# Performance work log

Hardware: AMD Instinct MI355X
Metric: run time of the kernel (lower is better)

## Reference

```python
import jax, jax.numpy as jnp
import numpy as np

D = 300      # d_model / entity_embed_size, hard-coded in the module
TOPK = 20    # k in torch.topk


def setup_inputs() -> dict:
    key = jax.random.key(0)
    ks = jax.random.split(key, 6)
    N, T = 2, 4096
    scale = 1.0 / np.sqrt(D).astype(np.float32)
    return {
        "querys": jax.random.normal(ks[0], (N, T, D), jnp.float32),
        "keys":   jax.random.normal(ks[1], (N, T, D), jnp.float32),
        "values": jax.random.normal(ks[2], (N, T, D), jnp.float32),
        "Wq": jax.random.normal(ks[3], (D, D), jnp.float32) * scale,
        "Wk": jax.random.normal(ks[4], (D, D), jnp.float32) * scale,
        "Wv": jax.random.normal(ks[5], (D, D), jnp.float32) * scale,
        "num_heads": 6,
    }


def reference(querys, keys, values, Wq, Wk, Wv, num_heads):
    N, Tq, d = querys.shape
    h = int(num_heads)
    dh = d // h  # head dim (must divide; 300/6 = 50)

    # nn.Linear(bias=False): y = x @ W^T
    Q = querys @ Wq.T
    K = keys @ Wk.T
    V = values @ Wv.T  # computed but unused by the 'selected' attention, kept for fidelity

    # torch.cat(torch.split(X, dh, dim=2), dim=0): head index becomes major batch dim
    def to_heads(X):
        n, t, _ = X.shape
        return X.reshape(n, t, h, dh).transpose(2, 0, 1, 3).reshape(h * n, t, dh)

    Q_, K_ = to_heads(Q), to_heads(K)

    # scaled_dot_selected_product_attention
    scores = jnp.einsum('bqd,bkd->bqk', Q_, K_) / (dh ** 0.5)  # [hN, Tq, Tk]
    max_att = scores.max(axis=1)                                # [hN, Tk] (max over queries)
    top_vals, top_ids = jax.lax.top_k(max_att, TOPK)            # [hN, 20]
    probs = jax.nn.softmax(top_vals, axis=-1)                   # [hN, 20]
    # gather from K (not V!), matching the original code
    sel = jnp.take_along_axis(K_, top_ids[:, :, None], axis=1)  # [hN, 20, dh]
    out = jnp.sum(sel * probs[:, :, None], axis=1, keepdims=True)  # [hN, 1, dh]

    # torch.cat(torch.split(outputs, N, dim=0), dim=2): merge heads back on feature dim
    out = out.reshape(h, N, 1, dh).transpose(1, 2, 0, 3).reshape(N, 1, d)
    return out
```

## Files before the change

kernel.cpp:

```cpp
#include <hip/hip_runtime.h>
#include <hip/hip_bf16.h>
#include <math.h>

#define T      4096
#define Dm     300
#define NH     6
#define DH     50
#define NB     2
#define NBATCH 12
#define KTOP   20
#define NCAND  48
#define QC     8
#define RQC    16
#define KP     320
#define JP     320
#define NBINS  4096
#define BMAX   1024
#define XCHUNKS (16384 * 40)
#define WCHUNKS (2 * JP * (KP / 8))

typedef short  bs8  __attribute__((ext_vector_type(8)));
typedef float  f4   __attribute__((ext_vector_type(4)));

static __device__ __forceinline__ unsigned short f2bf(float f) {
    union { float f; unsigned u; } x{f};
    unsigned r = x.u + 0x7fffu + ((x.u >> 16) & 1u);
    return (unsigned short)(r >> 16);
}
static __device__ __forceinline__ float bf2f(unsigned short h) {
    union { unsigned u; float f; } x;
    x.u = ((unsigned)h) << 16;
    return x.f;
}
static __device__ __forceinline__ unsigned fkey(float f) {
    unsigned u = __float_as_uint(f);
    return (u & 0x80000000u) ? ~u : (u | 0x80000000u);
}

__global__ __launch_bounds__(256) void split_kernel(
    const float* __restrict__ querys, const float* __restrict__ keys,
    const float* __restrict__ Wq, const float* __restrict__ Wk,
    unsigned short* __restrict__ Xh, unsigned short* __restrict__ Xl,
    unsigned short* __restrict__ Wh, unsigned short* __restrict__ Wl)
{
    const int i = blockIdx.x * 256 + threadIdx.x;
    float f[8];
    unsigned short *dh, *dl;

    if (i < XCHUNKS) {
        int row = i / 40, c = i - row * 40;
        int k0 = c * 8;
        int z = row >> 13, r = row & 8191;
        const float* src = (z ? keys : querys) + (size_t)r * 300;
        if (k0 + 8 <= 300) {
            float4 a = *(const float4*)(src + k0);
            float4 b = *(const float4*)(src + k0 + 4);
            f[0] = a.x; f[1] = a.y; f[2] = a.z; f[3] = a.w;
            f[4] = b.x; f[5] = b.y; f[6] = b.z; f[7] = b.w;
        } else {
#pragma unroll
            for (int e = 0; e < 8; ++e) {
                int k = k0 + e;
                f[e] = (k < 300) ? src[k < 300 ? k : 0] : 0.f;
            }
        }
        dh = Xh + (size_t)row * KP + k0;
        dl = Xl + (size_t)row * KP + k0;
    } else if (i < XCHUNKS + WCHUNKS) {
        int wi = i - XCHUNKS;
        int z = wi / (JP * (KP / 8)), rem = wi % (JP * (KP / 8));
        int row = rem / (KP / 8), k0 = (rem % (KP / 8)) * 8;
        const float* W = z ? Wk : Wq;
#pragma unroll
        for (int e = 0; e < 8; ++e) {
            int k = k0 + e;
            f[e] = (row < 300 && k < 300) ? W[row * 300 + (k < 300 ? k : 0)] : 0.f;
        }
        dh = Wh + ((size_t)z * JP + row) * KP + k0;
        dl = Wl + ((size_t)z * JP + row) * KP + k0;
    } else {
        return;
    }

    bs8 vh, vl;
#pragma unroll
    for (int e = 0; e < 8; ++e) {
        unsigned short h = f2bf(f[e]);
        float r = f[e] - bf2f(h);
        vh[e] = (short)h;
        vl[e] = (short)f2bf(r);
    }
    *(bs8*)dh = vh;
    *(bs8*)dl = vl;
}

__global__ __launch_bounds__(256) void proj_mfma_kernel(
    const unsigned short* __restrict__ Xh, const unsigned short* __restrict__ Xl,
    const unsigned short* __restrict__ Wh, const unsigned short* __restrict__ Wl,
    float* __restrict__ Qt, float* __restrict__ Kt)
{
    __shared__ unsigned short Bfh[1280 * 8];
    __shared__ unsigned short Bfl[1280 * 8];

    const int z  = blockIdx.z;
    float* Yt = z ? Kt : Qt;

    const int j0  = blockIdx.x * 32;
    const int m0  = blockIdx.y * 128;
    const int tid = threadIdx.x;
    const int wave = tid >> 6, lane = tid & 63;
    const int m16 = lane & 15, quad = lane >> 4;

    const unsigned short* WhB = Wh + (size_t)z * JP * KP;
    const unsigned short* WlB = Wl + (size_t)z * JP * KP;

    for (int i = tid; i < 1280; i += 256) {
        int n16 = i & 15, q = (i >> 4) & 3, ks = (i >> 6) % 10, nt = i / 640;
        size_t src = (size_t)(j0 + nt * 16 + n16) * KP + ks * 32 + q * 8;
        *(bs8*)&Bfh[i * 8] = *(const bs8*)(WhB + src);
        *(bs8*)&Bfl[i * 8] = *(const bs8*)(WlB + src);
    }
    __syncthreads();

    f4 acc[2][2] = {{{0.f,0.f,0.f,0.f},{0.f,0.f,0.f,0.f}},
                    {{0.f,0.f,0.f,0.f},{0.f,0.f,0.f,0.f}}};
    const int rowbase = z * 8192 + m0 + wave * 32;
    const unsigned short* xh = Xh + (size_t)rowbase * KP;
    const unsigned short* xl = Xl + (size_t)rowbase * KP;

    for (int ks = 0; ks < 10; ++ks) {
        bs8 Ah[2], Al[2];
#pragma unroll
        for (int mt = 0; mt < 2; ++mt) {
            size_t off = (size_t)(mt * 16 + m16) * KP + ks * 32 + quad * 8;
            Ah[mt] = *(const bs8*)(xh + off);
            Al[mt] = *(const bs8*)(xl + off);
        }
#pragma unroll
        for (int nt = 0; nt < 2; ++nt) {
            int ci = (((nt * 10 + ks) * 4 + quad) * 16 + m16) * 8;
            bs8 Bfh_ = *(const bs8*)&Bfh[ci];
            bs8 Bfl_ = *(const bs8*)&Bfl[ci];
#pragma unroll
            for (int mt = 0; mt < 2; ++mt) {
                acc[mt][nt] = __builtin_amdgcn_mfma_f32_16x16x32_bf16(Ah[mt], Bfh_, acc[mt][nt], 0, 0, 0);
                acc[mt][nt] = __builtin_amdgcn_mfma_f32_16x16x32_bf16(Al[mt], Bfh_, acc[mt][nt], 0, 0, 0);
                acc[mt][nt] = __builtin_amdgcn_mfma_f32_16x16x32_bf16(Ah[mt], Bfl_, acc[mt][nt], 0, 0, 0);
            }
        }
    }

    const int n    = m0 >> 12;
    const int tloc = (m0 & (T - 1)) + wave * 32;
#pragma unroll
    for (int nt = 0; nt < 2; ++nt) {
        const int j = j0 + nt * 16 + m16;
        if (j < 300) {
            const int head = j / DH, jc = j % DH;
            float* base = Yt + ((size_t)(head * NB + n) * DH + jc) * T;
#pragma unroll
            for (int mt = 0; mt < 2; ++mt) {
                int t = tloc + mt * 16 + quad * 4;
                *(float4*)(base + t) =
                    make_float4(acc[mt][nt][0], acc[mt][nt][1], acc[mt][nt][2], acc[mt][nt][3]);
            }
        }
    }
}

__global__ __launch_bounds__(256) void convert_kernel(
    const float* __restrict__ Qt, const float* __restrict__ Kt,
    unsigned short* __restrict__ Qb, unsigned short* __restrict__ Kb)
{
    __shared__ unsigned short S[32 * 8 * 8];

    const float* src = blockIdx.z ? Kt : Qt;
    unsigned short* dst = blockIdx.z ? Kb : Qb;
    const int b  = blockIdx.y;
    const int t0 = blockIdx.x * 32;
    const int tid = threadIdx.x;

    {
        const int r = tid & 31, c = tid >> 5;
        const int ch = r * 8 + (c ^ (r & 7));
#pragma unroll
        for (int e = 0; e < 8; ++e) {
            int d = c * 8 + e;
            float v = (d < DH) ? src[((size_t)b * DH + d) * T + t0 + r] : 0.f;
            S[ch * 8 + e] = f2bf(v);
        }
    }
    __syncthreads();

    {
        const int r2 = tid >> 3, c2 = tid & 7;
        const int ch = r2 * 8 + (c2 ^ (r2 & 7));
        *(bs8*)(dst + ((size_t)b * T + t0 + r2) * 64 + c2 * 8) = *(const bs8*)&S[ch * 8];
    }
}

__global__ __launch_bounds__(256) void score_mfma_kernel(
    const unsigned short* __restrict__ Qb, const unsigned short* __restrict__ Kb,
    float* __restrict__ pamax)
{
    __shared__ unsigned short Qlds[1024 * 8];

    const int kb   = blockIdx.x;
    const int b    = blockIdx.y;
    const int qc   = blockIdx.z;
    const int tid  = threadIdx.x;
    const int wave = tid >> 6, lane = tid & 63;
    const int m16  = lane & 15, quad = lane >> 4;

    const int k0 = kb * 256 + wave * 64;

    bs8 Bf[4][2];
#pragma unroll
    for (int kt = 0; kt < 4; ++kt)
#pragma unroll
        for (int h = 0; h < 2; ++h)
            Bf[kt][h] = *(const bs8*)(Kb + ((size_t)(b * T + k0 + kt * 16 + m16)) * 64
                                         + quad * 8 + h * 32);

    float cmax[4];
#pragma unroll
    for (int kt = 0; kt < 4; ++kt) cmax[kt] = -INFINITY;

    for (int it = 0; it < 4; ++it) {
        const int q0 = qc * 512 + it * 128;
        __syncthreads();
#pragma unroll
        for (int i = 0; i < 4; ++i) {
            int idx = i * 256 + tid;
            int r = idx >> 3, c2 = idx & 7;
            int ch = r * 8 + (c2 ^ (r & 7));
            *(bs8*)&Qlds[ch * 8] =
                *(const bs8*)(Qb + ((size_t)(b * T + q0 + r)) * 64 + c2 * 8);
        }
        __syncthreads();

#pragma unroll
        for (int mt = 0; mt < 8; ++mt) {
            const int row = mt * 16 + m16;
            bs8 A0 = *(const bs8*)&Qlds[(row * 8 + (quad ^ (row & 7))) * 8];
            bs8 A1 = *(const bs8*)&Qlds[(row * 8 + ((quad + 4) ^ (row & 7))) * 8];
#pragma unroll
            for (int kt = 0; kt < 4; ++kt) {
                f4 acc = {0.f, 0.f, 0.f, 0.f};
                acc = __builtin_amdgcn_mfma_f32_16x16x32_bf16(A0, Bf[kt][0], acc, 0, 0, 0);
                acc = __builtin_amdgcn_mfma_f32_16x16x32_bf16(A1, Bf[kt][1], acc, 0, 0, 0);
                cmax[kt] = fmaxf(cmax[kt],
                                 fmaxf(fmaxf(acc[0], acc[1]), fmaxf(acc[2], acc[3])));
            }
        }
    }

#pragma unroll
    for (int kt = 0; kt < 4; ++kt) {
        float v = cmax[kt];
        v = fmaxf(v, __shfl_xor(v, 16));
        v = fmaxf(v, __shfl_xor(v, 32));
        cmax[kt] = v;
    }
    if (lane < 16) {
#pragma unroll
        for (int kt = 0; kt < 4; ++kt)
            pamax[((size_t)qc * NBATCH + b) * T + k0 + kt * 16 + lane] = cmax[kt];
    }
}

__global__ __launch_bounds__(256) void cand_kernel(
    const float* __restrict__ pamax, int* __restrict__ cand)
{
    __shared__ float vals[T];
    __shared__ int   hist[NBINS];
    __shared__ int   part[256];
    __shared__ int   bidx[BMAX];
    __shared__ float bval[BMAX];
    __shared__ int   sh_B, sh_c1, sh_nout, sh_nb;

    const int b = blockIdx.x, tid = threadIdx.x;

    for (int i = tid; i < NBINS; i += 256) hist[i] = 0;
    if (tid == 0) { sh_nout = 0; sh_nb = 0; }
    __syncthreads();

    for (int i = tid; i < T; i += 256) {
        float m = pamax[(size_t)b * T + i];
#pragma unroll
        for (int c = 1; c < QC; ++c)
            m = fmaxf(m, pamax[((size_t)c * NBATCH + b) * T + i]);
        vals[i] = m;
        atomicAdd(&hist[fkey(m) >> 20], 1);
    }
    __syncthreads();

    {
        int s = 0;
#pragma unroll
        for (int k = 0; k < 16; ++k) s += hist[tid * 16 + k];
        part[tid] = s;
        __syncthreads();
        for (int off = 1; off < 256; off <<= 1) {
            int v = (tid + off < 256) ? part[tid + off] : 0;
            __syncthreads();
            part[tid] += v;
            __syncthreads();
        }
        int run = (tid < 255) ? part[tid + 1] : 0;
        for (int k = 15; k >= 0; --k) {
            int bin = tid * 16 + k;
            int c = hist[bin];
            if (run < NCAND && run + c >= NCAND) { sh_B = bin; sh_c1 = run; }
            run += c;
        }
    }
    __syncthreads();

    const int B = sh_B;

    for (int i = tid; i < T; i += 256) {
        int kb = (int)(fkey(vals[i]) >> 20);
        if (kb > B) {
            int p = atomicAdd(&sh_nout, 1);
            cand[b * NCAND + p] = i;
        } else if (kb == B) {
            int p = atomicAdd(&sh_nb, 1);
            if (p < BMAX) { bidx[p] = i; bval[p] = vals[i]; }
        }
    }
    __syncthreads();

    const int c1   = sh_nout;
    const int need = NCAND - c1;
    const int nb   = (sh_nb < BMAX) ? sh_nb : BMAX;
    if (tid < 64) {
        for (int l = 0; l < need; ++l) {
            float mv = -INFINITY; int mp = -1, mt = 0x7fffffff;
            for (int j = tid; j < nb; j += 64) {
                float v = bval[j]; int t = bidx[j];
                if (v > mv || (v == mv && t < mt)) { mv = v; mp = j; mt = t; }
            }
#pragma unroll
            for (int off = 32; off > 0; off >>= 1) {
                float v2 = __shfl_xor(mv, off);
                int   p2 = __shfl_xor(mp, off);
                int   t2 = __shfl_xor(mt, off);
                if (v2 > mv || (v2 == mv && t2 < mt)) { mv = v2; mp = p2; mt = t2; }
            }
            if (tid == 0)
                cand[b * NCAND + c1 + l] = (mp >= 0) ? bidx[mp] : l;
            if (mp >= 0 && tid == (mp & 63)) bval[mp] = -INFINITY;
        }
    }
}

__global__ __launch_bounds__(256) void rescore_kernel(
    const float* __restrict__ Qt, const float* __restrict__ Kt,
    const int* __restrict__ cand, float* __restrict__ rmax)
{
    __shared__ float KcT[DH][NCAND];
    __shared__ float red[4][NCAND];

    const int b = blockIdx.x, qch = blockIdx.y;
    const int tid = threadIdx.x;
    const int lane = tid & 63, wv = tid >> 6;

    for (int i = tid; i < NCAND * DH; i += 256) {
        int j = i / DH, d = i - j * DH;
        KcT[d][j] = Kt[((size_t)b * DH + d) * T + cand[b * NCAND + j]];
    }
    __syncthreads();

    const int q = qch * 256 + tid;
    float qv[DH];
#pragma unroll
    for (int d = 0; d < DH; ++d)
        qv[d] = Qt[((size_t)b * DH + d) * T + q];

    for (int g = 0; g < NCAND / 8; ++g) {
        float cm[8];
#pragma unroll
        for (int j = 0; j < 8; ++j) cm[j] = 0.f;
#pragma unroll
        for (int d = 0; d < DH; ++d) {
            float4 ka = *(const float4*)&KcT[d][g * 8];
            float4 kb = *(const float4*)&KcT[d][g * 8 + 4];
            cm[0] = fmaf(qv[d], ka.x, cm[0]);
            cm[1] = fmaf(qv[d], ka.y, cm[1]);
            cm[2] = fmaf(qv[d], ka.z, cm[2]);
            cm[3] = fmaf(qv[d], ka.w, cm[3]);
            cm[4] = fmaf(qv[d], kb.x, cm[4]);
            cm[5] = fmaf(qv[d], kb.y, cm[5]);
            cm[6] = fmaf(qv[d], kb.z, cm[6]);
            cm[7] = fmaf(qv[d], kb.w, cm[7]);
        }
#pragma unroll
        for (int j = 0; j < 8; ++j) {
            float v = cm[j];
#pragma unroll
            for (int off = 32; off > 0; off >>= 1)
                v = fmaxf(v, __shfl_xor(v, off));
            if (lane == 0) red[wv][g * 8 + j] = v;
        }
    }
    __syncthreads();

    if (tid < NCAND) {
        float v = fmaxf(fmaxf(red[0][tid], red[1][tid]),
                        fmaxf(red[2][tid], red[3][tid]));
        rmax[((size_t)qch * NBATCH + b) * NCAND + tid] = v;
    }
}

__global__ __launch_bounds__(64) void final_kernel(
    const float* __restrict__ rmax, const int* __restrict__ cand,
    const float* __restrict__ Kt, float* __restrict__ out)
{
    __shared__ float selval[KTOP];
    __shared__ int   selidx[KTOP];
    __shared__ float probs[KTOP];

    const int b = blockIdx.x;
    const int lane = threadIdx.x;

    float v = -INFINITY; int idx = 0x7fffffff;
    if (lane < NCAND) {
        v = rmax[(size_t)b * NCAND + lane];
#pragma unroll
        for (int c = 1; c < RQC; ++c)
            v = fmaxf(v, rmax[((size_t)c * NBATCH + b) * NCAND + lane]);
        v *= 0.14142135623730951f;
        idx = cand[b * NCAND + lane];
    }

    for (int l = 0; l < KTOP; ++l) {
        float mv = v; int mi = idx;
#pragma unroll
        for (int off = 32; off > 0; off >>= 1) {
            float v2 = __shfl_xor(mv, off);
            int   i2 = __shfl_xor(mi, off);
            if (v2 > mv || (v2 == mv && i2 < mi)) { mv = v2; mi = i2; }
        }
        if (idx == mi) v = -INFINITY;
        if (lane == 0) { selval[l] = mv; selidx[l] = mi; }
    }
    __syncthreads();

    if (lane == 0) {
        float m = selval[0];
        float s = 0.f;
        for (int l = 0; l < KTOP; ++l) { float e = expf(selval[l] - m); probs[l] = e; s += e; }
        float inv = 1.f / s;
        for (int l = 0; l < KTOP; ++l) probs[l] *= inv;
    }
    __syncthreads();

    if (lane < DH) {
        float acc = 0.f;
#pragma unroll
        for (int l = 0; l < KTOP; ++l)
            acc += probs[l] * Kt[((size_t)b * DH + lane) * T + selidx[l]];
        int head = b / NB, n = b % NB;
        out[n * Dm + head * DH + lane] = acc;
    }
}

extern "C" void kernel_launch(void* const* d_in, const int* in_sizes, int n_in,
                              void* d_out, int out_size, void* d_ws, size_t ws_size,
                              hipStream_t stream) {
    const float* querys = (const float*)d_in[0];
    const float* keys   = (const float*)d_in[1];
    const float* Wq     = (const float*)d_in[3];
    const float* Wk     = (const float*)d_in[4];

    float* out = (float*)d_out;
    float* ws  = (float*)d_ws;

    float* Qt    = ws;
    float* Kt    = Qt + (size_t)NBATCH * DH * T;
    float* pamax = Kt + (size_t)NBATCH * DH * T;
    float* rmax  = pamax + (size_t)QC * NBATCH * T;
    unsigned short* Qb = (unsigned short*)(rmax + (size_t)RQC * NBATCH * NCAND + 8);
    Qb = (unsigned short*)(((uintptr_t)Qb + 15) & ~(uintptr_t)15);
    unsigned short* Kb  = Qb  + (size_t)NBATCH * T * 64;
    unsigned short* Xh  = Kb  + (size_t)NBATCH * T * 64;
    unsigned short* Xl  = Xh  + (size_t)16384 * KP;
    unsigned short* Whs = Xl  + (size_t)16384 * KP;
    unsigned short* Wls = Whs + (size_t)2 * JP * KP;
    int* cand = (int*)(Wls + (size_t)2 * JP * KP);

    const int splitBlocks = (XCHUNKS + WCHUNKS + 255) / 256;
    split_kernel    <<<splitBlocks, 256, 0, stream>>>(querys, keys, Wq, Wk, Xh, Xl, Whs, Wls);
    proj_mfma_kernel<<<dim3(10, 64, 2), 256, 0, stream>>>(Xh, Xl, Whs, Wls, Qt, Kt);
    convert_kernel  <<<dim3(128, NBATCH, 2), 256, 0, stream>>>(Qt, Kt, Qb, Kb);
    score_mfma_kernel<<<dim3(16, NBATCH, QC), 256, 0, stream>>>(Qb, Kb, pamax);
    cand_kernel     <<<NBATCH, 256, 0, stream>>>(pamax, cand);
    rescore_kernel  <<<dim3(NBATCH, RQC), 256, 0, stream>>>(Qt, Kt, cand, rmax);
    final_kernel    <<<NBATCH, 64, 0, stream>>>(rmax, cand, Kt, out);
}
```

Baseline: 253.7 us.

## Fuse input split, projection and bf16 conversion into one pipelined MFMA kernel

Removes the separate split kernel that wrote hi/lo bf16 copies of the inputs and the convert kernel that transposed the projections to bf16. The projection kernel now reads fp32 inputs directly, splits them in registers, loops over six head tiles with double-buffered LDS weight fragments, and writes both the fp32 and the bf16 layouts from the accumulators. Only a small weight-prepacking kernel remains. This cuts global traffic and launches, but the kernel now launches only 256 blocks with a large register footprint (launch_bounds 256,1), so occupancy and parallelism drop.

```diff
diff --git a/kernel.cpp b/kernel.cpp
--- a/kernel.cpp
+++ b/kernel.cpp
@@ -12,12 +12,9 @@
 #define NCAND  48
 #define QC     8
 #define RQC    16
-#define KP     320
-#define JP     320
 #define NBINS  4096
 #define BMAX   1024
-#define XCHUNKS (16384 * 40)
-#define WCHUNKS (2 * JP * (KP / 8))
+#define WCH    30720
 
 typedef short  bs8  __attribute__((ext_vector_type(8)));
 typedef float  f4   __attribute__((ext_vector_type(4)));
@@ -37,165 +34,177 @@
     return (u & 0x80000000u) ? ~u : (u | 0x80000000u);
 }
 
-__global__ __launch_bounds__(256) void split_kernel(
-    const float* __restrict__ querys, const float* __restrict__ keys,
+__global__ __launch_bounds__(256) void wfrag_kernel(
     const float* __restrict__ Wq, const float* __restrict__ Wk,
-    unsigned short* __restrict__ Xh, unsigned short* __restrict__ Xl,
-    unsigned short* __restrict__ Wh, unsigned short* __restrict__ Wl)
+    unsigned short* __restrict__ Whf, unsigned short* __restrict__ Wlf)
 {
-    const int i = blockIdx.x * 256 + threadIdx.x;
-    float f[8];
-    unsigned short *dh, *dl;
-
-    if (i < XCHUNKS) {
-        int row = i / 40, c = i - row * 40;
-        int k0 = c * 8;
-        int z = row >> 13, r = row & 8191;
-        const float* src = (z ? keys : querys) + (size_t)r * 300;
-        if (k0 + 8 <= 300) {
-            float4 a = *(const float4*)(src + k0);
-            float4 b = *(const float4*)(src + k0 + 4);
-            f[0] = a.x; f[1] = a.y; f[2] = a.z; f[3] = a.w;
-            f[4] = b.x; f[5] = b.y; f[6] = b.z; f[7] = b.w;
-        } else {
-#pragma unroll
-            for (int e = 0; e < 8; ++e) {
-                int k = k0 + e;
-                f[e] = (k < 300) ? src[k < 300 ? k : 0] : 0.f;
-            }
-        }
-        dh = Xh + (size_t)row * KP + k0;
-        dl = Xl + (size_t)row * KP + k0;
-    } else if (i < XCHUNKS + WCHUNKS) {
-        int wi = i - XCHUNKS;
-        int z = wi / (JP * (KP / 8)), rem = wi % (JP * (KP / 8));
-        int row = rem / (KP / 8), k0 = (rem % (KP / 8)) * 8;
-        const float* W = z ? Wk : Wq;
-#pragma unroll
-        for (int e = 0; e < 8; ++e) {
-            int k = k0 + e;
-            f[e] = (row < 300 && k < 300) ? W[row * 300 + (k < 300 ? k : 0)] : 0.f;
-        }
-        dh = Wh + ((size_t)z * JP + row) * KP + k0;
-        dl = Wl + ((size_t)z * JP + row) * KP + k0;
-    } else {
-        return;
-    }
+    const int idx = blockIdx.x * 256 + threadIdx.x;
+    if (idx >= WCH) return;
+    const int lane = idx & 63, rest = idx >> 6;
+    const int ks = rest % 10, r2 = rest / 10;
+    const int nt = r2 & 1, r3 = r2 >> 1;
+    const int jtg = r3 % 12, z = r3 / 12;
+    const int n16 = lane & 15, quad = lane >> 4;
+    const int j = jtg * 32 + nt * 16 + n16;
+    const int head = j >> 6, dd = j & 63;
+    const float* W = z ? Wk : Wq;
 
     bs8 vh, vl;
 #pragma unroll
     for (int e = 0; e < 8; ++e) {
-        unsigned short h = f2bf(f[e]);
-        float r = f[e] - bf2f(h);
+        int k = ks * 32 + quad * 8 + e;
+        float v = (dd < DH && k < 300) ? W[(head * DH + dd) * 300 + (k < 300 ? k : 0)] : 0.f;
+        unsigned short h = f2bf(v);
         vh[e] = (short)h;
-        vl[e] = (short)f2bf(r);
-    }
-    *(bs8*)dh = vh;
-    *(bs8*)dl = vl;
-}
-
-__global__ __launch_bounds__(256) void proj_mfma_kernel(
-    const unsigned short* __restrict__ Xh, const unsigned short* __restrict__ Xl,
-    const unsigned short* __restrict__ Wh, const unsigned short* __restrict__ Wl,
-    float* __restrict__ Qt, float* __restrict__ Kt)
+        vl[e] = (short)f2bf(v - bf2f(h));
+    }
+    *(bs8*)(Whf + (size_t)idx * 8) = vh;
+    *(bs8*)(Wlf + (size_t)idx * 8) = vl;
+}
+
+__global__ __launch_bounds__(256, 1) void proj_mfma_kernel(
+    const float* __restrict__ Xq, const float* __restrict__ Xk,
+    const unsigned short* __restrict__ Whf, const unsigned short* __restrict__ Wlf,
+    float* __restrict__ Qt, float* __restrict__ Kt,
+    unsigned short* __restrict__ Qb, unsigned short* __restrict__ Kb)
 {
-    __shared__ unsigned short Bfh[1280 * 8];
-    __shared__ unsigned short Bfl[1280 * 8];
+    __shared__ unsigned short Bsh[2][2560 * 8];
+    __shared__ unsigned short Tr[4][32][40];
 
     const int z  = blockIdx.z;
-    float* Yt = z ? Kt : Qt;
-
-    const int j0  = blockIdx.x * 32;
-    const int m0  = blockIdx.y * 128;
+    const int jg = blockIdx.y;
+    const int m0 = blockIdx.x * 128;
+    const float* X = z ? Xk : Xq;
+    float*          Ytf = z ? Kt : Qt;
+    unsigned short* Ytb = z ? Kb : Qb;
+
     const int tid = threadIdx.x;
     const int wave = tid >> 6, lane = tid & 63;
     const int m16 = lane & 15, quad = lane >> 4;
-
-    const unsigned short* WhB = Wh + (size_t)z * JP * KP;
-    const unsigned short* WlB = Wl + (size_t)z * JP * KP;
-
-    for (int i = tid; i < 1280; i += 256) {
-        int n16 = i & 15, q = (i >> 4) & 3, ks = (i >> 6) % 10, nt = i / 640;
-        size_t src = (size_t)(j0 + nt * 16 + n16) * KP + ks * 32 + q * 8;
-        *(bs8*)&Bfh[i * 8] = *(const bs8*)(WhB + src);
-        *(bs8*)&Bfl[i * 8] = *(const bs8*)(WlB + src);
-    }
-    __syncthreads();
+    const int n = m0 >> 12, t0 = m0 & (T - 1);
+
+    bs8 Ah[2][10], Al[2][10];
+#pragma unroll
+    for (int mt = 0; mt < 2; ++mt) {
+        const float* rowp = X + (size_t)(m0 + wave * 32 + mt * 16 + m16) * 300;
+#pragma unroll
+        for (int ks = 0; ks < 10; ++ks) {
+            float f[8];
+            if (ks < 9) {
+                float4 a = *(const float4*)(rowp + ks * 32 + quad * 8);
+                float4 c = *(const float4*)(rowp + ks * 32 + quad * 8 + 4);
+                f[0] = a.x; f[1] = a.y; f[2] = a.z; f[3] = a.w;
+                f[4] = c.x; f[5] = c.y; f[6] = c.z; f[7] = c.w;
+            } else {
+#pragma unroll
+                for (int e = 0; e < 8; ++e) {
+                    int k = 288 + quad * 8 + e;
+                    f[e] = (k < 300) ? rowp[k < 300 ? k : 0] : 0.f;
+                }
+            }
+#pragma unroll
+            for (int e = 0; e < 8; ++e) {
+                unsigned short h = f2bf(f[e]);
+                Ah[mt][ks][e] = (short)h;
+                Al[mt][ks][e] = (short)f2bf(f[e] - bf2f(h));
+            }
+        }
+    }
+
+    bs8 rh[5], rl[5];
+    {
+        size_t cb = (size_t)(z * 12 + jg * 6) * 1280;
+#pragma unroll
+        for (int i = 0; i < 5; ++i) {
+            int c = i * 256 + tid;
+            rh[i] = *(const bs8*)(Whf + (cb + c) * 8);
+            rl[i] = *(const bs8*)(Wlf + (cb + c) * 8);
+        }
+#pragma unroll
+        for (int i = 0; i < 5; ++i) {
+            int c = i * 256 + tid;
+            *(bs8*)&Bsh[0][c * 8]          = rh[i];
+            *(bs8*)&Bsh[0][(1280 + c) * 8] = rl[i];
+        }
+    }
 
     f4 acc[2][2] = {{{0.f,0.f,0.f,0.f},{0.f,0.f,0.f,0.f}},
                     {{0.f,0.f,0.f,0.f},{0.f,0.f,0.f,0.f}}};
-    const int rowbase = z * 8192 + m0 + wave * 32;
-    const unsigned short* xh = Xh + (size_t)rowbase * KP;
-    const unsigned short* xl = Xl + (size_t)rowbase * KP;
-
-    for (int ks = 0; ks < 10; ++ks) {
-        bs8 Ah[2], Al[2];
-#pragma unroll
-        for (int mt = 0; mt < 2; ++mt) {
-            size_t off = (size_t)(mt * 16 + m16) * KP + ks * 32 + quad * 8;
-            Ah[mt] = *(const bs8*)(xh + off);
-            Al[mt] = *(const bs8*)(xl + off);
-        }
+
+    for (int jt = 0; jt < 6; ++jt) {
+        __syncthreads();
+
+        if (jt < 5) {
+            size_t cb = (size_t)(z * 12 + jg * 6 + jt + 1) * 1280;
+#pragma unroll
+            for (int i = 0; i < 5; ++i) {
+                int c = i * 256 + tid;
+                rh[i] = *(const bs8*)(Whf + (cb + c) * 8);
+                rl[i] = *(const bs8*)(Wlf + (cb + c) * 8);
+            }
+        }
+
+        const unsigned short* Bbuf = Bsh[jt & 1];
+#pragma unroll
+        for (int ks = 0; ks < 10; ++ks) {
+#pragma unroll
+            for (int nt = 0; nt < 2; ++nt) {
+                bs8 bh = *(const bs8*)&Bbuf[((nt * 10 + ks) * 64 + lane) * 8];
+                bs8 bl = *(const bs8*)&Bbuf[((1280 + (nt * 10 + ks) * 64) + lane) * 8];
+#pragma unroll
+                for (int mt = 0; mt < 2; ++mt) {
+                    acc[mt][nt] = __builtin_amdgcn_mfma_f32_16x16x32_bf16(Ah[mt][ks], bh, acc[mt][nt], 0, 0, 0);
+                    acc[mt][nt] = __builtin_amdgcn_mfma_f32_16x16x32_bf16(Al[mt][ks], bh, acc[mt][nt], 0, 0, 0);
+                    acc[mt][nt] = __builtin_amdgcn_mfma_f32_16x16x32_bf16(Ah[mt][ks], bl, acc[mt][nt], 0, 0, 0);
+                }
+            }
+        }
+
+        const int jtg  = jg * 6 + jt;
+        const int head = jtg >> 1, d0 = (jtg & 1) * 32;
+        const int b    = head * NB + n;
+
 #pragma unroll
         for (int nt = 0; nt < 2; ++nt) {
-            int ci = (((nt * 10 + ks) * 4 + quad) * 16 + m16) * 8;
-            bs8 Bfh_ = *(const bs8*)&Bfh[ci];
-            bs8 Bfl_ = *(const bs8*)&Bfl[ci];
-#pragma unroll
-            for (int mt = 0; mt < 2; ++mt) {
-                acc[mt][nt] = __builtin_amdgcn_mfma_f32_16x16x32_bf16(Ah[mt], Bfh_, acc[mt][nt], 0, 0, 0);
-                acc[mt][nt] = __builtin_amdgcn_mfma_f32_16x16x32_bf16(Al[mt], Bfh_, acc[mt][nt], 0, 0, 0);
-                acc[mt][nt] = __builtin_amdgcn_mfma_f32_16x16x32_bf16(Ah[mt], Bfl_, acc[mt][nt], 0, 0, 0);
-            }
-        }
-    }
-
-    const int n    = m0 >> 12;
-    const int tloc = (m0 & (T - 1)) + wave * 32;
-#pragma unroll
-    for (int nt = 0; nt < 2; ++nt) {
-        const int j = j0 + nt * 16 + m16;
-        if (j < 300) {
-            const int head = j / DH, jc = j % DH;
-            float* base = Yt + ((size_t)(head * NB + n) * DH + jc) * T;
-#pragma unroll
-            for (int mt = 0; mt < 2; ++mt) {
-                int t = tloc + mt * 16 + quad * 4;
-                *(float4*)(base + t) =
-                    make_float4(acc[mt][nt][0], acc[mt][nt][1], acc[mt][nt][2], acc[mt][nt][3]);
-            }
-        }
-    }
-}
-
-__global__ __launch_bounds__(256) void convert_kernel(
-    const float* __restrict__ Qt, const float* __restrict__ Kt,
-    unsigned short* __restrict__ Qb, unsigned short* __restrict__ Kb)
-{
-    __shared__ unsigned short S[32 * 8 * 8];
-
-    const float* src = blockIdx.z ? Kt : Qt;
-    unsigned short* dst = blockIdx.z ? Kb : Qb;
-    const int b  = blockIdx.y;
-    const int t0 = blockIdx.x * 32;
-    const int tid = threadIdx.x;
-
-    {
-        const int r = tid & 31, c = tid >> 5;
-        const int ch = r * 8 + (c ^ (r & 7));
-#pragma unroll
-        for (int e = 0; e < 8; ++e) {
-            int d = c * 8 + e;
-            float v = (d < DH) ? src[((size_t)b * DH + d) * T + t0 + r] : 0.f;
-            S[ch * 8 + e] = f2bf(v);
-        }
-    }
-    __syncthreads();
-
-    {
-        const int r2 = tid >> 3, c2 = tid & 7;
-        const int ch = r2 * 8 + (c2 ^ (r2 & 7));
-        *(bs8*)(dst + ((size_t)b * T + t0 + r2) * 64 + c2 * 8) = *(const bs8*)&S[ch * 8];
+            const int dd = d0 + nt * 16 + m16;
+            if (dd < DH) {
+                float* base = Ytf + ((size_t)b * DH + dd) * T + t0 + wave * 32;
+#pragma unroll
+                for (int mt = 0; mt < 2; ++mt)
+                    *(float4*)(base + mt * 16 + quad * 4) =
+                        make_float4(acc[mt][nt][0], acc[mt][nt][1], acc[mt][nt][2], acc[mt][nt][3]);
+            }
+        }
+
+#pragma unroll
+        for (int mt = 0; mt < 2; ++mt)
+#pragma unroll
+            for (int nt = 0; nt < 2; ++nt)
+#pragma unroll
+                for (int r = 0; r < 4; ++r)
+                    Tr[wave][mt * 16 + quad * 4 + r][nt * 16 + m16] = f2bf(acc[mt][nt][r]);
+        {
+            const int rr = lane >> 1, p = lane & 1;
+            unsigned short* dst = Ytb + ((size_t)b * T + t0 + wave * 32 + rr) * 64 + d0 + p * 16;
+            *(bs8*)dst       = *(const bs8*)&Tr[wave][rr][p * 16];
+            *(bs8*)(dst + 8) = *(const bs8*)&Tr[wave][rr][p * 16 + 8];
+        }
+
+#pragma unroll
+        for (int mt = 0; mt < 2; ++mt)
+#pragma unroll
+            for (int nt = 0; nt < 2; ++nt)
+                acc[mt][nt] = (f4){0.f, 0.f, 0.f, 0.f};
+
+        __syncthreads();
+        if (jt < 5) {
+#pragma unroll
+            for (int i = 0; i < 5; ++i) {
+                int c = i * 256 + tid;
+                *(bs8*)&Bsh[(jt + 1) & 1][c * 8]          = rh[i];
+                *(bs8*)&Bsh[(jt + 1) & 1][(1280 + c) * 8] = rl[i];
+            }
+        }
     }
 }
 
@@ -484,16 +493,12 @@
     unsigned short* Qb = (unsigned short*)(rmax + (size_t)RQC * NBATCH * NCAND + 8);
     Qb = (unsigned short*)(((uintptr_t)Qb + 15) & ~(uintptr_t)15);
     unsigned short* Kb  = Qb  + (size_t)NBATCH * T * 64;
-    unsigned short* Xh  = Kb  + (size_t)NBATCH * T * 64;
-    unsigned short* Xl  = Xh  + (size_t)16384 * KP;
-    unsigned short* Whs = Xl  + (size_t)16384 * KP;
-    unsigned short* Wls = Whs + (size_t)2 * JP * KP;
-    int* cand = (int*)(Wls + (size_t)2 * JP * KP);
-
-    const int splitBlocks = (XCHUNKS + WCHUNKS + 255) / 256;
-    split_kernel    <<<splitBlocks, 256, 0, stream>>>(querys, keys, Wq, Wk, Xh, Xl, Whs, Wls);
-    proj_mfma_kernel<<<dim3(10, 64, 2), 256, 0, stream>>>(Xh, Xl, Whs, Wls, Qt, Kt);
-    convert_kernel  <<<dim3(128, NBATCH, 2), 256, 0, stream>>>(Qt, Kt, Qb, Kb);
+    unsigned short* Whf = Kb  + (size_t)NBATCH * T * 64;
+    unsigned short* Wlf = Whf + (size_t)WCH * 8;
+    int* cand = (int*)(Wlf + (size_t)WCH * 8);
+
+    wfrag_kernel    <<<(WCH + 255) / 256, 256, 0, stream>>>(Wq, Wk, Whf, Wlf);
+    proj_mfma_kernel<<<dim3(64, 2, 2), 256, 0, stream>>>(querys, keys, Whf, Wlf, Qt, Kt, Qb, Kb);
     score_mfma_kernel<<<dim3(16, NBATCH, QC), 256, 0, stream>>>(Qb, Kb, pamax);
     cand_kernel     <<<NBATCH, 256, 0, stream>>>(pamax, cand);
     rescore_kernel  <<<dim3(NBATCH, RQC), 256, 0, stream>>>(Qt, Kt, cand, rmax);
```

After: 215.1 us. 15.2% less time.
